# Optimization experiments

Measured on AMD Instinct MI355X. Metric: run time of the kernel, lower is better.

## Reference

```python
import jax, jax.numpy as jnp
import numpy as np
from jax import lax

ALPHA = 0.5
GAMMA = 0.01
BIG = 1e8  # stands in for +inf boundary of the soft-DTW DP table


def _softmin3(a, b, c, gamma):
    x = jnp.stack([a, b, c], axis=0)
    return -gamma * jax.nn.logsumexp(-x / gamma, axis=0)


def _softdtw_values(D, gamma):
    """Soft-DTW values for a batch of cost matrices.

    D: [M, N, N] pairwise cost matrices -> [M] soft-DTW values R[N, N].
    Computed with an anti-diagonal lax.scan (2N-1 sequential steps), fully
    vectorized over the batch and over each diagonal.
    """
    M, N, _ = D.shape
    Dpad = jnp.zeros((M, N + 1, N + 1), D.dtype).at[:, 1:, 1:].set(D)
    ii = jnp.arange(N + 1)
    # diagonal d=0: only R[0,0]=0 ; diagonal d=1: R[0,1]=R[1,0]=inf
    prev2 = jnp.full((M, N + 1), BIG, D.dtype).at[:, 0].set(0.0)
    prev1 = jnp.full((M, N + 1), BIG, D.dtype)

    def shift(r):  # r at index i-1, BIG at i=0
        return jnp.concatenate([jnp.full((M, 1), BIG, r.dtype), r[:, :-1]], axis=1)

    def step(carry, d):
        p2, p1 = carry
        j = d - ii
        valid = (ii >= 1) & (ii <= N) & (j >= 1) & (j <= N)
        jc = jnp.clip(j, 0, N)
        dvals = Dpad[:, ii, jc]  # [M, N+1] costs on this diagonal
        # R[i,j] = D[i,j] + softmin(R[i-1,j-1], R[i-1,j], R[i,j-1])
        smin = _softmin3(shift(p2), shift(p1), p1, gamma)
        cur = jnp.where(valid[None, :], dvals + smin, BIG)
        return (p1, cur), None

    (_, cur), _ = lax.scan(step, (prev2, prev1), jnp.arange(2, 2 * N + 1))
    return cur[:, N]  # R[N, N]


def setup_inputs() -> dict:
    key = jax.random.key(0)
    k1, k2 = jax.random.split(key)
    outputs = jax.random.normal(k1, (64, 128, 4), dtype=jnp.float32)
    targets = jax.random.normal(k2, (64, 128, 4), dtype=jnp.float32)
    return {"outputs": outputs, "targets": targets}


def reference(outputs, targets):
    B, T, C = outputs.shape
    # Per (sample, channel): D[i, j] = (target_i - output_j)^2  (rows = target idx)
    t = jnp.transpose(targets, (0, 2, 1)).reshape(B * C, T)
    o = jnp.transpose(outputs, (0, 2, 1)).reshape(B * C, T)
    D = (t[:, :, None] - o[:, None, :]) ** 2  # [B*C, T, T]

    # shape loss: mean over batch of soft-DTW values, summed over channels
    vals = _softdtw_values(D, GAMMA)  # [B*C]
    loss_shape = vals.sum() / B

    # temporal loss: soft alignment path E = d(softDTW)/dD, penalized by (i-j)^2
    path = jax.grad(lambda DD: _softdtw_values(DD, GAMMA).sum())(D)  # [B*C, T, T]
    idx = jnp.arange(1, T + 1, dtype=D.dtype)
    Omega = (idx[:, None] - idx[None, :]) ** 2  # [T, T]
    loss_temporal = (path * Omega).sum() / (B * T * T)

    return ALPHA * loss_shape + (1.0 - ALPHA) * loss_temporal
```

## Files before the change

kernel.cpp:

```cpp
#include <hip/hip_runtime.h>


#define TN 128
#define BATCH 64
#define CH 4
#define KCH 8

__device__ __forceinline__ float fast_exp2(float x) { return __builtin_amdgcn_exp2f(x); }
__device__ __forceinline__ float fast_log2(float x) { return __builtin_amdgcn_logf(x); }
__device__ __forceinline__ float fast_rcp(float x)  { return __builtin_amdgcn_rcpf(x); }

__device__ __forceinline__ float dpp_shr1(float x, float fill) {
  union { float f; int i; } o, s, r;
  o.f = fill; s.f = x;
  r.i = __builtin_amdgcn_update_dpp(o.i, s.i, 0x138, 0xF, 0xF, false);
  return r.f;
}

__global__ __launch_bounds__(128)
void dilate_softdtw_kernel(const float* __restrict__ outputs,
                           const float* __restrict__ targets,
                           float* __restrict__ out) {
  __shared__ float obuf[384];
  __shared__ float2 Bb[192];
  __shared__ int prog;

  const float WALLP = -4.328085e6f;
  const float O_PAD = 15.0f;
  const float K2    = 144.2695040888963f;

  const int m = blockIdx.x, b = m >> 2, c = m & 3;
  const int tid  = threadIdx.x;
  const int wid  = tid >> 6;
  const int lane = tid & 63;

  const float* tb = targets + (size_t)b*(TN*CH) + c;
  const float* ob = outputs + (size_t)b*(TN*CH) + c;

  #pragma unroll
  for (int s = 0; s < 3; ++s) {
    const int idx = tid + 128*s;
    const int k = idx - 126;
    obuf[idx] = ((unsigned)k <= 127u) ? ob[k*CH] : O_PAD;
  }
  const float t0 = tb[(wid*64 + lane)*CH];
  if (tid == 0) prog = 0;
  __syncthreads();

  const float* oc = obuf + 126;

  if (wid == 0) {
    float p1  = WALLP;
    float up2 = (lane == 0) ? 0.0f : WALLP;
    float dp1 = 0.f, dup2 = 0.f;
    float fd  = (float)(2*lane);
    float o0  = oc[-lane];

    #pragma unroll 4
    for (int d = 2; d <= 192; ++d) {
      const int j0 = d - 1 - lane;
      const float o_nxt = oc[j0];
      float up1  = dpp_shr1(p1, WALLP);
      float dup1 = dpp_shr1(dp1, 0.f);

      float mn = fmaxf(up2, fmaxf(up1, p1));
      float a = up2 - mn, bq = up1 - mn, cc = p1 - mn;
      float ea = fast_exp2(a);
      float eb = fast_exp2(bq);
      float ec = fast_exp2(cc);
      float sum = (ea + eb) + ec;
      float rs = fast_rcp(sum);
      float l  = fast_log2(sum);
      float df = t0 - o0;
      float q  = df*df;
      float jv = __builtin_fmaf(ea, dup2, __builtin_fmaf(eb, dup1, ec*dp1));
      float w  = fd*fd;
      float cv = __builtin_fmaf(-K2, q, mn + l);
      float dv = __builtin_fmaf(rs, jv, w);

      if (lane == 63) Bb[d - 1] = make_float2(cv, dv);
      if (((d - 1) & (KCH - 1)) == 0) {
        if (lane == 63)
          __hip_atomic_store(&prog, d, __ATOMIC_RELEASE, __HIP_MEMORY_SCOPE_WORKGROUP);
      }

      up2 = up1; p1 = cv; dup2 = dup1; dp1 = dv;
      o0 = o_nxt; fd -= 1.0f;
    }
    if (lane == 63)
      __hip_atomic_store(&prog, 1000, __ATOMIC_RELEASE, __HIP_MEMORY_SCOPE_WORKGROUP);
  } else {
    float p1  = WALLP, up2 = WALLP;
    float dp1 = 0.f, dup2 = 0.f;
    float fd  = (float)(64 + 2*lane);
    float o0  = oc[-lane];
    float2 bc;
    bool first = true;

    for (int d0 = 66; d0 <= 256; d0 += KCH) {
      int target = d0 + KCH - 1;
      if (target > 185) target = 1000;
      while (__hip_atomic_load(&prog, __ATOMIC_ACQUIRE, __HIP_MEMORY_SCOPE_WORKGROUP) < target) {}
      if (first) { bc = Bb[64]; first = false; }

      const int dend = (d0 + KCH - 1 < 256) ? d0 + KCH - 1 : 256;
      #pragma unroll 4
      for (int d = d0; d <= dend; ++d) {
        const int j0 = d - 65 - lane;
        const float o_nxt = oc[j0];
        const int bi = (d - 1 > 191) ? 191 : (d - 1);
        const float2 bn = Bb[bi];
        float up1  = dpp_shr1(p1, bc.x);
        float dup1 = dpp_shr1(dp1, bc.y);

        float mn = fmaxf(up2, fmaxf(up1, p1));
        float a = up2 - mn, bq = up1 - mn, cc = p1 - mn;
        float ea = fast_exp2(a);
        float eb = fast_exp2(bq);
        float ec = fast_exp2(cc);
        float sum = (ea + eb) + ec;
        float rs = fast_rcp(sum);
        float l  = fast_log2(sum);
        float df = t0 - o0;
        float q  = df*df;
        float jv = __builtin_fmaf(ea, dup2, __builtin_fmaf(eb, dup1, ec*dp1));
        float w  = fd*fd;
        float cv = __builtin_fmaf(-K2, q, mn + l);
        float dv = __builtin_fmaf(rs, jv, w);

        up2 = up1; p1 = cv; dup2 = dup1; dp1 = dv;
        o0 = o_nxt; fd -= 1.0f; bc = bn;
      }
    }

    if (lane == 63) {
      const float partial = __builtin_fmaf(p1, -5.415212348e-5f,
                                           dp1 * 4.76837158203125e-7f);
      atomicAdd(out, partial);
    }
  }
}

extern "C" void kernel_launch(void* const* d_in, const int* in_sizes, int n_in,
                              void* d_out, int out_size, void* d_ws, size_t ws_size,
                              hipStream_t stream) {
  const float* outputs = (const float*)d_in[0];
  const float* targets = (const float*)d_in[1];
  float* out = (float*)d_out;
  (void)in_sizes; (void)n_in; (void)out_size; (void)d_ws; (void)ws_size;

  (void)hipMemsetAsync(out, 0, sizeof(float), stream);
  dilate_softdtw_kernel<<<dim3(256), dim3(128), 0, stream>>>(outputs, targets, out);
}
```

Baseline: 82.81 us.

## Pack two soft-DTW sequences per block and fully unroll consumer chunk loop

Each block now runs two independent (sample, channel) sequences, each with its own producer/consumer wavefront pair, shared buffers and progress flag, so the grid shrinks to 128 blocks of 256 threads. The consumer wavefront's inner chunk loop is fully unrolled with fixed bounds. The clamped boundary index is replaced by a padded Bb region filled with wall values. The aim is to remove per-step bounds logic and improve scheduling by co-locating wavefronts, at the cost of fewer blocks spread across the CUs.

```diff
diff --git a/kernel.cpp b/kernel.cpp
--- a/kernel.cpp
+++ b/kernel.cpp
@@ -17,39 +17,44 @@
   return r.f;
 }
 
-__global__ __launch_bounds__(128)
+__global__ __launch_bounds__(256)
 void dilate_softdtw_kernel(const float* __restrict__ outputs,
                            const float* __restrict__ targets,
                            float* __restrict__ out) {
-  __shared__ float obuf[384];
-  __shared__ float2 Bb[192];
-  __shared__ int prog;
+  __shared__ float obuf[2][384];
+  __shared__ float2 Bb[2][256];
+  __shared__ int prog[2];
 
   const float WALLP = -4.328085e6f;
   const float O_PAD = 15.0f;
   const float K2    = 144.2695040888963f;
 
-  const int m = blockIdx.x, b = m >> 2, c = m & 3;
   const int tid  = threadIdx.x;
   const int wid  = tid >> 6;
   const int lane = tid & 63;
+  const int seq  = wid & 1;
+  const int half = wid >> 1;
 
+  const int m = blockIdx.x * 2 + seq, b = m >> 2, c = m & 3;
   const float* tb = targets + (size_t)b*(TN*CH) + c;
   const float* ob = outputs + (size_t)b*(TN*CH) + c;
 
+  const int lid = half*64 + lane;
   #pragma unroll
   for (int s = 0; s < 3; ++s) {
-    const int idx = tid + 128*s;
+    const int idx = lid + 128*s;
     const int k = idx - 126;
-    obuf[idx] = ((unsigned)k <= 127u) ? ob[k*CH] : O_PAD;
+    obuf[seq][idx] = ((unsigned)k <= 127u) ? ob[k*CH] : O_PAD;
   }
-  const float t0 = tb[(wid*64 + lane)*CH];
-  if (tid == 0) prog = 0;
+  if (half == 1) Bb[seq][192 + lane] = make_float2(WALLP, 0.f);
+  const float t0 = tb[(half*64 + lane)*CH];
+  if (lid == 0) prog[seq] = 0;
   __syncthreads();
 
-  const float* oc = obuf + 126;
+  const float* oc = obuf[seq] + 126;
+  int* pp = &prog[seq];
 
-  if (wid == 0) {
+  if (half == 0) {
     float p1  = WALLP;
     float up2 = (lane == 0) ? 0.0f : WALLP;
     float dp1 = 0.f, dup2 = 0.f;
@@ -78,60 +83,60 @@
       float cv = __builtin_fmaf(-K2, q, mn + l);
       float dv = __builtin_fmaf(rs, jv, w);
 
-      if (lane == 63) Bb[d - 1] = make_float2(cv, dv);
+      if (lane == 63) Bb[seq][d - 1] = make_float2(cv, dv);
       if (((d - 1) & (KCH - 1)) == 0) {
         if (lane == 63)
-          __hip_atomic_store(&prog, d, __ATOMIC_RELEASE, __HIP_MEMORY_SCOPE_WORKGROUP);
+          __hip_atomic_store(pp, d, __ATOMIC_RELEASE, __HIP_MEMORY_SCOPE_WORKGROUP);
       }
 
       up2 = up1; p1 = cv; dup2 = dup1; dp1 = dv;
       o0 = o_nxt; fd -= 1.0f;
     }
     if (lane == 63)
-      __hip_atomic_store(&prog, 1000, __ATOMIC_RELEASE, __HIP_MEMORY_SCOPE_WORKGROUP);
+      __hip_atomic_store(pp, 1000, __ATOMIC_RELEASE, __HIP_MEMORY_SCOPE_WORKGROUP);
   } else {
     float p1  = WALLP, up2 = WALLP;
     float dp1 = 0.f, dup2 = 0.f;
     float fd  = (float)(64 + 2*lane);
     float o0  = oc[-lane];
-    float2 bc;
-    bool first = true;
 
-    for (int d0 = 66; d0 <= 256; d0 += KCH) {
-      int target = d0 + KCH - 1;
-      if (target > 185) target = 1000;
-      while (__hip_atomic_load(&prog, __ATOMIC_ACQUIRE, __HIP_MEMORY_SCOPE_WORKGROUP) < target) {}
-      if (first) { bc = Bb[64]; first = false; }
+    auto cstep = [&](int d, float2& bc) {
+      const int j0 = d - 65 - lane;
+      const float o_nxt = oc[j0];
+      const float2 bn = Bb[seq][d - 1];
+      float up1  = dpp_shr1(p1, bc.x);
+      float dup1 = dpp_shr1(dp1, bc.y);
 
-      const int dend = (d0 + KCH - 1 < 256) ? d0 + KCH - 1 : 256;
-      #pragma unroll 4
-      for (int d = d0; d <= dend; ++d) {
-        const int j0 = d - 65 - lane;
-        const float o_nxt = oc[j0];
-        const int bi = (d - 1 > 191) ? 191 : (d - 1);
-        const float2 bn = Bb[bi];
-        float up1  = dpp_shr1(p1, bc.x);
-        float dup1 = dpp_shr1(dp1, bc.y);
+      float mn = fmaxf(up2, fmaxf(up1, p1));
+      float a = up2 - mn, bq = up1 - mn, cc = p1 - mn;
+      float ea = fast_exp2(a);
+      float eb = fast_exp2(bq);
+      float ec = fast_exp2(cc);
+      float sum = (ea + eb) + ec;
+      float rs = fast_rcp(sum);
+      float l  = fast_log2(sum);
+      float df = t0 - o0;
+      float q  = df*df;
+      float jv = __builtin_fmaf(ea, dup2, __builtin_fmaf(eb, dup1, ec*dp1));
+      float w  = fd*fd;
+      float cv = __builtin_fmaf(-K2, q, mn + l);
+      float dv = __builtin_fmaf(rs, jv, w);
 
-        float mn = fmaxf(up2, fmaxf(up1, p1));
-        float a = up2 - mn, bq = up1 - mn, cc = p1 - mn;
-        float ea = fast_exp2(a);
-        float eb = fast_exp2(bq);
-        float ec = fast_exp2(cc);
-        float sum = (ea + eb) + ec;
-        float rs = fast_rcp(sum);
-        float l  = fast_log2(sum);
-        float df = t0 - o0;
-        float q  = df*df;
-        float jv = __builtin_fmaf(ea, dup2, __builtin_fmaf(eb, dup1, ec*dp1));
-        float w  = fd*fd;
-        float cv = __builtin_fmaf(-K2, q, mn + l);
-        float dv = __builtin_fmaf(rs, jv, w);
+      up2 = up1; p1 = cv; dup2 = dup1; dp1 = dv;
+      o0 = o_nxt; fd -= 1.0f; bc = bn;
+    };
 
-        up2 = up1; p1 = cv; dup2 = dup1; dp1 = dv;
-        o0 = o_nxt; fd -= 1.0f; bc = bn;
-      }
+    while (__hip_atomic_load(pp, __ATOMIC_ACQUIRE, __HIP_MEMORY_SCOPE_WORKGROUP) < 73) {}
+    float2 bc = Bb[seq][64];
+    for (int d0 = 66; d0 <= 178; d0 += KCH) {
+      const int target = d0 + KCH - 1;
+      while (__hip_atomic_load(pp, __ATOMIC_ACQUIRE, __HIP_MEMORY_SCOPE_WORKGROUP) < target) {}
+      #pragma unroll
+      for (int k = 0; k < KCH; ++k) cstep(d0 + k, bc);
     }
+    while (__hip_atomic_load(pp, __ATOMIC_ACQUIRE, __HIP_MEMORY_SCOPE_WORKGROUP) < 1000) {}
+    #pragma unroll 4
+    for (int d = 186; d <= 256; ++d) cstep(d, bc);
 
     if (lane == 63) {
       const float partial = __builtin_fmaf(p1, -5.415212348e-5f,
@@ -150,5 +155,5 @@
   (void)in_sizes; (void)n_in; (void)out_size; (void)d_ws; (void)ws_size;
 
   (void)hipMemsetAsync(out, 0, sizeof(float), stream);
-  dilate_softdtw_kernel<<<dim3(256), dim3(128), 0, stream>>>(outputs, targets, out);
+  dilate_softdtw_kernel<<<dim3(128), dim3(256), 0, stream>>>(outputs, targets, out);
 }
```

Measured after the change: 76.54 us, median of 2. 7.6% less time.
